# Kernel optimization log

Hardware: AMD Instinct MI355X
Metric: run time of the kernel (lower is better)

Reference implementation:

```python
import jax, jax.numpy as jnp
import numpy as np
import math

B, Z, D = 1024, 32768, 128

def setup_inputs() -> dict:
    key = jax.random.key(0)
    k1, k2, k3 = jax.random.split(key, 3)
    z_sparse = jax.random.randint(k1, (B, Z), 0, 2, dtype=jnp.int32)
    context_embedding = jax.random.normal(k2, (B, D), dtype=jnp.float32)
    embd_table = jax.random.normal(k3, (Z, D), dtype=jnp.float32)  # nn.Embedding weight
    return {"z_sparse": z_sparse, "context_embedding": context_embedding, "embd_table": embd_table}

def reference(z_sparse, context_embedding, embd_table):
    # mask[b, z] = feature z active in batch b  (matches (z_sparse > 0).nonzero())
    mask = z_sparse > 0  # [B, Z]
    # attn_scores = (ctx * emb).sum(-1) / sqrt(D), densified over all (b, z)
    scores = (context_embedding @ embd_table.T) / math.sqrt(embd_table.shape[1])  # [B, Z]
    # per-batch softmax over active features only
    masked = jnp.where(mask, scores, -jnp.inf)
    w = jax.nn.softmax(masked, axis=-1)
    w = jnp.where(mask, w, 0.0)  # zero inactive (also kills NaN for all-empty rows)
    # scatter-add of emb * weight == weighted matmul against the table
    out = w @ embd_table  # [B, D]
    counts = jnp.clip(jnp.sum(mask, axis=-1), 1, None)  # bincount(...).clamp(min=1)
    return out / counts[:, None].astype(out.dtype)
```

## Files before the change

kernel.cpp:

```cpp
#include <hip/hip_runtime.h>
#include <stdint.h>

#define B_SZ 1024
#define Z_SZ 32768
#define D_SZ 128
#define NZ   32
#define CZ   (Z_SZ / NZ)
#define TZ   64
#define ITERS (CZ / TZ)
#define TBLK 64
#define WROWS 16

#define SEMB_STRIDE  136
#define SEMBT_STRIDE 72
#define SP_STRIDE    72

#define WS_O   0
#define WS_M   (NZ * B_SZ * D_SZ)
#define WS_L   (WS_M + NZ * B_SZ)
#define WS_C   (WS_L + NZ * B_SZ)

typedef short bf16x8 __attribute__((ext_vector_type(8)));
typedef float f32x4  __attribute__((ext_vector_type(4)));

__device__ __forceinline__ unsigned short f2bf(float f) {
    union { float f; uint32_t u; } v; v.f = f;
    uint32_t u = v.u;
    u = (u + 0x7FFFu + ((u >> 16) & 1u)) >> 16;
    return (unsigned short)u;
}

__global__ __launch_bounds__(256, 2) void attn_part(
    const int*   __restrict__ zs,
    const float* __restrict__ ctx,
    const float* __restrict__ emb,
    float*       __restrict__ ws)
{
    __shared__ __align__(16) unsigned short s_emb [TZ   * SEMB_STRIDE];
    __shared__ __align__(16) unsigned short s_embT[D_SZ * SEMBT_STRIDE];
    __shared__ __align__(16) unsigned short s_P   [4 * WROWS * SP_STRIDE];

    const int tid  = threadIdx.x;
    const int wave = tid >> 6;
    const int lane = tid & 63;
    const int l15  = lane & 15;
    const int quad = lane >> 4;

    const int bg     = blockIdx.x;
    const int ch     = blockIdx.y;
    const int z_base = ch * CZ;
    const int wb0    = bg * TBLK + wave * WROWS;

    bf16x8 afrag[4];
    {
        const float scale = 0.08838834764831845f;
        const float* crow = ctx + (size_t)(wb0 + l15) * D_SZ;
#pragma unroll
        for (int ks = 0; ks < 4; ++ks) {
            const float* p = crow + ks * 32 + quad * 8;
            float4 x0 = *(const float4*)(p);
            float4 x1 = *(const float4*)(p + 4);
            bf16x8 a;
            a[0] = (short)f2bf(x0.x * scale); a[1] = (short)f2bf(x0.y * scale);
            a[2] = (short)f2bf(x0.z * scale); a[3] = (short)f2bf(x0.w * scale);
            a[4] = (short)f2bf(x1.x * scale); a[5] = (short)f2bf(x1.y * scale);
            a[6] = (short)f2bf(x1.z * scale); a[7] = (short)f2bf(x1.w * scale);
            afrag[ks] = a;
        }
    }

    float m_r[4], l_r[4];
    int   cnt_r[4];
    f32x4 acc2[8];
#pragma unroll
    for (int r = 0; r < 4; ++r) { m_r[r] = -1e30f; l_r[r] = 0.f; cnt_r[r] = 0; }
#pragma unroll
    for (int n = 0; n < 8; ++n) { acc2[n][0]=0.f; acc2[n][1]=0.f; acc2[n][2]=0.f; acc2[n][3]=0.f; }

    for (int it = 0; it < ITERS; ++it) {
        const int z0 = z_base + it * TZ;

        __syncthreads();

        {
            const int r  = tid >> 2;
            const int q3 = tid & 3;
            const float* erow = emb + (size_t)(z0 + r) * D_SZ + q3 * 32;
            unsigned short* dst = s_emb + r * SEMB_STRIDE + q3 * 32;
#pragma unroll
            for (int u = 0; u < 8; ++u) {
                float4 x = *(const float4*)(erow + 4 * u);
                ushort4 h;
                h.x = f2bf(x.x); h.y = f2bf(x.y); h.z = f2bf(x.z); h.w = f2bf(x.w);
                *(ushort4*)(dst + 4 * u) = h;
            }
        }
        {
            const int d  = tid & 127;
            const int zh = tid >> 7;
            const float* ecol = emb + (size_t)(z0 + zh * 32) * D_SZ + d;
            unsigned short* dst = s_embT + d * SEMBT_STRIDE + zh * 32;
#pragma unroll
            for (int g = 0; g < 4; ++g) {
                float v0 = ecol[(8*g + 0) * D_SZ]; float v1 = ecol[(8*g + 1) * D_SZ];
                float v2 = ecol[(8*g + 2) * D_SZ]; float v3 = ecol[(8*g + 3) * D_SZ];
                float v4 = ecol[(8*g + 4) * D_SZ]; float v5 = ecol[(8*g + 5) * D_SZ];
                float v6 = ecol[(8*g + 6) * D_SZ]; float v7 = ecol[(8*g + 7) * D_SZ];
                ushort2 h;
                h.x = f2bf(v0); h.y = f2bf(v1); *(ushort2*)(dst + 8*g + 0) = h;
                h.x = f2bf(v2); h.y = f2bf(v3); *(ushort2*)(dst + 8*g + 2) = h;
                h.x = f2bf(v4); h.y = f2bf(v5); *(ushort2*)(dst + 8*g + 4) = h;
                h.x = f2bf(v6); h.y = f2bf(v7); *(ushort2*)(dst + 8*g + 6) = h;
            }
        }

        int msk[4][4];
#pragma unroll
        for (int r = 0; r < 4; ++r) {
            const int b = wb0 + quad * 4 + r;
            const int* p = zs + (size_t)b * Z_SZ + z0 + l15;
#pragma unroll
            for (int nt = 0; nt < 4; ++nt) msk[nt][r] = (p[nt * 16] > 0) ? 1 : 0;
            cnt_r[r] += msk[0][r] + msk[1][r] + msk[2][r] + msk[3][r];
        }

        __syncthreads();

        f32x4 sfr[4];
#pragma unroll
        for (int nt = 0; nt < 4; ++nt) {
            f32x4 c; c[0]=0.f; c[1]=0.f; c[2]=0.f; c[3]=0.f;
            const unsigned short* bb = s_emb + (nt * 16 + l15) * SEMB_STRIDE + quad * 8;
#pragma unroll
            for (int ks = 0; ks < 4; ++ks) {
                bf16x8 bf = *(const bf16x8*)(bb + ks * 32);
                c = __builtin_amdgcn_mfma_f32_16x16x32_bf16(afrag[ks], bf, c, 0, 0, 0);
            }
            sfr[nt] = c;
        }

        float tmax[4];
#pragma unroll
        for (int r = 0; r < 4; ++r) {
            float a0 = msk[0][r] ? sfr[0][r] : -1e30f;
            float a1 = msk[1][r] ? sfr[1][r] : -1e30f;
            float a2 = msk[2][r] ? sfr[2][r] : -1e30f;
            float a3 = msk[3][r] ? sfr[3][r] : -1e30f;
            tmax[r] = fmaxf(fmaxf(a0, a1), fmaxf(a2, a3));
        }
#pragma unroll
        for (int s = 1; s < 16; s <<= 1) {
#pragma unroll
            for (int r = 0; r < 4; ++r) tmax[r] = fmaxf(tmax[r], __shfl_xor(tmax[r], s));
        }
        float alpha[4];
#pragma unroll
        for (int r = 0; r < 4; ++r) {
            float mnew = fmaxf(m_r[r], tmax[r]);
            alpha[r] = __expf(m_r[r] - mnew);
            m_r[r] = mnew;
            l_r[r] *= alpha[r];
        }
        float psum[4]; psum[0]=0.f; psum[1]=0.f; psum[2]=0.f; psum[3]=0.f;
        unsigned short* pw = s_P + wave * (WROWS * SP_STRIDE);
#pragma unroll
        for (int nt = 0; nt < 4; ++nt) {
#pragma unroll
            for (int r = 0; r < 4; ++r) {
                float p = msk[nt][r] ? __expf(sfr[nt][r] - m_r[r]) : 0.f;
                psum[r] += p;
                pw[(quad * 4 + r) * SP_STRIDE + nt * 16 + l15] = f2bf(p);
            }
        }
#pragma unroll
        for (int s = 1; s < 16; s <<= 1) {
#pragma unroll
            for (int r = 0; r < 4; ++r) psum[r] += __shfl_xor(psum[r], s);
        }
#pragma unroll
        for (int r = 0; r < 4; ++r) l_r[r] += psum[r];

#pragma unroll
        for (int n = 0; n < 8; ++n) {
#pragma unroll
            for (int r = 0; r < 4; ++r) acc2[n][r] *= alpha[r];
        }

        const unsigned short* pb = pw + l15 * SP_STRIDE + quad * 8;
        bf16x8 pA0 = *(const bf16x8*)(pb);
        bf16x8 pA1 = *(const bf16x8*)(pb + 32);
#pragma unroll
        for (int nt2 = 0; nt2 < 8; ++nt2) {
            const unsigned short* tb = s_embT + (nt2 * 16 + l15) * SEMBT_STRIDE + quad * 8;
            bf16x8 b0 = *(const bf16x8*)(tb);
            bf16x8 b1 = *(const bf16x8*)(tb + 32);
            acc2[nt2] = __builtin_amdgcn_mfma_f32_16x16x32_bf16(pA0, b0, acc2[nt2], 0, 0, 0);
            acc2[nt2] = __builtin_amdgcn_mfma_f32_16x16x32_bf16(pA1, b1, acc2[nt2], 0, 0, 0);
        }
    }

#pragma unroll
    for (int nt2 = 0; nt2 < 8; ++nt2) {
#pragma unroll
        for (int r = 0; r < 4; ++r) {
            const int b = wb0 + quad * 4 + r;
            ws[WS_O + ((size_t)ch * B_SZ + b) * D_SZ + nt2 * 16 + l15] = acc2[nt2][r];
        }
    }
    float cntf[4];
#pragma unroll
    for (int r = 0; r < 4; ++r) cntf[r] = (float)cnt_r[r];
#pragma unroll
    for (int s = 1; s < 16; s <<= 1) {
#pragma unroll
        for (int r = 0; r < 4; ++r) cntf[r] += __shfl_xor(cntf[r], s);
    }
    if (l15 == 0) {
#pragma unroll
        for (int r = 0; r < 4; ++r) {
            const int b = wb0 + quad * 4 + r;
            ws[WS_M + ch * B_SZ + b] = m_r[r];
            ws[WS_L + ch * B_SZ + b] = l_r[r];
            ws[WS_C + ch * B_SZ + b] = cntf[r];
        }
    }
}

__global__ __launch_bounds__(128) void attn_reduce(
    const float* __restrict__ ws, float* __restrict__ out)
{
    const int b = blockIdx.x;
    const int d = threadIdx.x;
    const float* mP = ws + WS_M;
    const float* lP = ws + WS_L;
    const float* cP = ws + WS_C;

    float M = -1e30f;
#pragma unroll
    for (int c = 0; c < NZ; ++c) M = fmaxf(M, mP[c * B_SZ + b]);

    float L = 0.f, C = 0.f, acc = 0.f;
#pragma unroll
    for (int c = 0; c < NZ; ++c) {
        float w = __expf(mP[c * B_SZ + b] - M);
        L += lP[c * B_SZ + b] * w;
        C += cP[c * B_SZ + b];
        acc += ws[WS_O + ((size_t)c * B_SZ + b) * D_SZ + d] * w;
    }
    float cnt = fmaxf(C, 1.0f);
    out[(size_t)b * D_SZ + d] = (L > 0.f) ? acc / (L * cnt) : 0.f;
}

extern "C" void kernel_launch(void* const* d_in, const int* in_sizes, int n_in,
                              void* d_out, int out_size, void* d_ws, size_t ws_size,
                              hipStream_t stream) {
    (void)in_sizes; (void)n_in; (void)out_size; (void)ws_size;
    const int*   zs  = (const int*)  d_in[0];
    const float* ctx = (const float*)d_in[1];
    const float* emb = (const float*)d_in[2];
    float* out = (float*)d_out;
    float* ws  = (float*)d_ws;

    dim3 grid1(B_SZ / TBLK, NZ);
    attn_part<<<grid1, 256, 0, stream>>>(zs, ctx, emb, ws);
    attn_reduce<<<B_SZ, 128, 0, stream>>>(ws, out);
}
```

Measured before the change: 248.1 us.

## Precompute bf16 embedding table and transpose once, read MFMA operands from global

```diff
diff --git a/kernel.cpp b/kernel.cpp
--- a/kernel.cpp
+++ b/kernel.cpp
@@ -11,14 +11,14 @@
 #define TBLK 64
 #define WROWS 16
 
-#define SEMB_STRIDE  136
-#define SEMBT_STRIDE 72
 #define SP_STRIDE    72
 
-#define WS_O   0
-#define WS_M   (NZ * B_SZ * D_SZ)
-#define WS_L   (WS_M + NZ * B_SZ)
-#define WS_C   (WS_L + NZ * B_SZ)
+#define WS_O    0
+#define WS_M    (NZ * B_SZ * D_SZ)
+#define WS_L    (WS_M + NZ * B_SZ)
+#define WS_C    (WS_L + NZ * B_SZ)
+#define WS_EB_F (WS_C + NZ * B_SZ)
+#define WS_ET_F (WS_EB_F + (Z_SZ * D_SZ / 2))
 
 typedef short bf16x8 __attribute__((ext_vector_type(8)));
 typedef float f32x4  __attribute__((ext_vector_type(4)));
@@ -30,15 +30,47 @@
     return (unsigned short)u;
 }
 
+__global__ __launch_bounds__(256) void convert_emb(
+    const float* __restrict__ emb,
+    unsigned short* __restrict__ embB,
+    unsigned short* __restrict__ embT)
+{
+    __shared__ unsigned short s[128 * 68];
+    const int tid = threadIdx.x;
+    const int z0  = blockIdx.x * 64;
+    const int zl  = tid >> 2;
+    const int ds  = (tid & 3) * 32;
+    const float* src = emb + (size_t)(z0 + zl) * D_SZ + ds;
+    unsigned short* dstB = embB + (size_t)(z0 + zl) * D_SZ + ds;
+#pragma unroll
+    for (int u = 0; u < 8; ++u) {
+        float4 x = *(const float4*)(src + 4 * u);
+        ushort4 h; h.x = f2bf(x.x); h.y = f2bf(x.y); h.z = f2bf(x.z); h.w = f2bf(x.w);
+        *(ushort4*)(dstB + 4 * u) = h;
+        s[(ds + 4*u + 0) * 68 + zl] = h.x;
+        s[(ds + 4*u + 1) * 68 + zl] = h.y;
+        s[(ds + 4*u + 2) * 68 + zl] = h.z;
+        s[(ds + 4*u + 3) * 68 + zl] = h.w;
+    }
+    __syncthreads();
+    const int d  = tid >> 1;
+    const int zh = (tid & 1) * 32;
+    unsigned short* dstT = embT + (size_t)d * Z_SZ + z0 + zh;
+    const unsigned short* srow = s + d * 68 + zh;
+#pragma unroll
+    for (int u = 0; u < 8; ++u) {
+        *(ushort4*)(dstT + 4 * u) = *(const ushort4*)(srow + 4 * u);
+    }
+}
+
 __global__ __launch_bounds__(256, 2) void attn_part(
-    const int*   __restrict__ zs,
-    const float* __restrict__ ctx,
-    const float* __restrict__ emb,
-    float*       __restrict__ ws)
+    const int*            __restrict__ zs,
+    const float*          __restrict__ ctx,
+    const unsigned short* __restrict__ embB,
+    const unsigned short* __restrict__ embT,
+    float*                __restrict__ ws)
 {
-    __shared__ __align__(16) unsigned short s_emb [TZ   * SEMB_STRIDE];
-    __shared__ __align__(16) unsigned short s_embT[D_SZ * SEMBT_STRIDE];
-    __shared__ __align__(16) unsigned short s_P   [4 * WROWS * SP_STRIDE];
+    __shared__ __align__(16) unsigned short s_P[4 * WROWS * SP_STRIDE];
 
     const int tid  = threadIdx.x;
     const int wave = tid >> 6;
@@ -77,43 +109,11 @@
 #pragma unroll
     for (int n = 0; n < 8; ++n) { acc2[n][0]=0.f; acc2[n][1]=0.f; acc2[n][2]=0.f; acc2[n][3]=0.f; }
 
+    unsigned short* pw = s_P + wave * (WROWS * SP_STRIDE);
+
     for (int it = 0; it < ITERS; ++it) {
         const int z0 = z_base + it * TZ;
 
-        __syncthreads();
-
-        {
-            const int r  = tid >> 2;
-            const int q3 = tid & 3;
-            const float* erow = emb + (size_t)(z0 + r) * D_SZ + q3 * 32;
-            unsigned short* dst = s_emb + r * SEMB_STRIDE + q3 * 32;
-#pragma unroll
-            for (int u = 0; u < 8; ++u) {
-                float4 x = *(const float4*)(erow + 4 * u);
-                ushort4 h;
-                h.x = f2bf(x.x); h.y = f2bf(x.y); h.z = f2bf(x.z); h.w = f2bf(x.w);
-                *(ushort4*)(dst + 4 * u) = h;
-            }
-        }
-        {
-            const int d  = tid & 127;
-            const int zh = tid >> 7;
-            const float* ecol = emb + (size_t)(z0 + zh * 32) * D_SZ + d;
-            unsigned short* dst = s_embT + d * SEMBT_STRIDE + zh * 32;
-#pragma unroll
-            for (int g = 0; g < 4; ++g) {
-                float v0 = ecol[(8*g + 0) * D_SZ]; float v1 = ecol[(8*g + 1) * D_SZ];
-                float v2 = ecol[(8*g + 2) * D_SZ]; float v3 = ecol[(8*g + 3) * D_SZ];
-                float v4 = ecol[(8*g + 4) * D_SZ]; float v5 = ecol[(8*g + 5) * D_SZ];
-                float v6 = ecol[(8*g + 6) * D_SZ]; float v7 = ecol[(8*g + 7) * D_SZ];
-                ushort2 h;
-                h.x = f2bf(v0); h.y = f2bf(v1); *(ushort2*)(dst + 8*g + 0) = h;
-                h.x = f2bf(v2); h.y = f2bf(v3); *(ushort2*)(dst + 8*g + 2) = h;
-                h.x = f2bf(v4); h.y = f2bf(v5); *(ushort2*)(dst + 8*g + 4) = h;
-                h.x = f2bf(v6); h.y = f2bf(v7); *(ushort2*)(dst + 8*g + 6) = h;
-            }
-        }
-
         int msk[4][4];
 #pragma unroll
         for (int r = 0; r < 4; ++r) {
@@ -124,13 +124,11 @@
             cnt_r[r] += msk[0][r] + msk[1][r] + msk[2][r] + msk[3][r];
         }
 
-        __syncthreads();
-
         f32x4 sfr[4];
 #pragma unroll
         for (int nt = 0; nt < 4; ++nt) {
             f32x4 c; c[0]=0.f; c[1]=0.f; c[2]=0.f; c[3]=0.f;
-            const unsigned short* bb = s_emb + (nt * 16 + l15) * SEMB_STRIDE + quad * 8;
+            const unsigned short* bb = embB + (size_t)(z0 + nt * 16 + l15) * D_SZ + quad * 8;
 #pragma unroll
             for (int ks = 0; ks < 4; ++ks) {
                 bf16x8 bf = *(const bf16x8*)(bb + ks * 32);
@@ -162,7 +160,6 @@
             l_r[r] *= alpha[r];
         }
         float psum[4]; psum[0]=0.f; psum[1]=0.f; psum[2]=0.f; psum[3]=0.f;
-        unsigned short* pw = s_P + wave * (WROWS * SP_STRIDE);
 #pragma unroll
         for (int nt = 0; nt < 4; ++nt) {
 #pragma unroll
@@ -191,7 +188,7 @@
         bf16x8 pA1 = *(const bf16x8*)(pb + 32);
 #pragma unroll
         for (int nt2 = 0; nt2 < 8; ++nt2) {
-            const unsigned short* tb = s_embT + (nt2 * 16 + l15) * SEMBT_STRIDE + quad * 8;
+            const unsigned short* tb = embT + (size_t)(nt2 * 16 + l15) * Z_SZ + z0 + quad * 8;
             bf16x8 b0 = *(const bf16x8*)(tb);
             bf16x8 b1 = *(const bf16x8*)(tb + 32);
             acc2[nt2] = __builtin_amdgcn_mfma_f32_16x16x32_bf16(pA0, b0, acc2[nt2], 0, 0, 0);
@@ -226,11 +223,11 @@
     }
 }
 
-__global__ __launch_bounds__(128) void attn_reduce(
+__global__ __launch_bounds__(256) void attn_reduce(
     const float* __restrict__ ws, float* __restrict__ out)
 {
-    const int b = blockIdx.x;
-    const int d = threadIdx.x;
+    const int b = blockIdx.x * 2 + (threadIdx.x >> 7);
+    const int d = threadIdx.x & 127;
     const float* mP = ws + WS_M;
     const float* lP = ws + WS_L;
     const float* cP = ws + WS_C;
@@ -261,7 +258,13 @@
     float* out = (float*)d_out;
     float* ws  = (float*)d_ws;
 
+    unsigned short* embB = (unsigned short*)(ws + WS_EB_F);
+    unsigned short* embT = (unsigned short*)(ws + WS_ET_F);
+
+    convert_emb<<<Z_SZ / 64, 256, 0, stream>>>(emb, embB, embT);
+
     dim3 grid1(B_SZ / TBLK, NZ);
-    attn_part<<<grid1, 256, 0, stream>>>(zs, ctx, emb, ws);
-    attn_reduce<<<B_SZ, 128, 0, stream>>>(ws, out);
-}
+    attn_part<<<grid1, 256, 0, stream>>>(zs, ctx, embB, embT, ws);
+
+    attn_reduce<<<B_SZ / 2, 256, 0, stream>>>(ws, out);
+}
```

After: 407.9 us. 1.64x slower.
